# Performance work log

Hardware: AMD Instinct MI355X
Metric: run time of the kernel (lower is better)

## Reference

```python
import jax, jax.numpy as jnp
import numpy as np

B, S, E, H = 2, 2048, 1024, 16
D = E // H  # head_dim = 64


def setup_inputs() -> dict:
    key = jax.random.key(0)
    ks = jax.random.split(key, 5)
    return {
        "hidden_states": jax.random.normal(ks[0], (B, S, E), jnp.float32),
        "c_attn_w": jax.random.normal(ks[1], (E, 3 * E), jnp.float32) * 0.02,
        "c_attn_b": jnp.zeros((3 * E,), jnp.float32),
        "c_proj_w": jax.random.normal(ks[2], (E, E), jnp.float32) * 0.02,
        "c_proj_b": jnp.zeros((E,), jnp.float32),
    }


def reference(hidden_states, c_attn_w, c_attn_b, c_proj_w, c_proj_b):
    # Conv1D: x @ w + b -> qkv [B, S, 3E]
    qkv = hidden_states @ c_attn_w + c_attn_b
    q, k, v = jnp.split(qkv, 3, axis=-1)
    # [B, H, S, D]
    q = q.reshape(B, S, H, D).transpose(0, 2, 1, 3)
    k = k.reshape(B, S, H, D).transpose(0, 2, 1, 3)
    v = v.reshape(B, S, H, D).transpose(0, 2, 1, 3)
    # scores [B, H, S, S], scaled by sqrt(head_dim)
    scores = jnp.einsum("bhqd,bhkd->bhqk", q, k) / jnp.sqrt(jnp.asarray(D, q.dtype))
    causal = jnp.tril(jnp.ones((S, S), bool))  # [S, S]
    mask_value = jnp.finfo(scores.dtype).min
    scores = jnp.where(causal, scores, mask_value)
    attn = jax.nn.softmax(scores, axis=-1)
    # attn @ V -> [B, H, S, D] -> [B, S, E]
    out = jnp.einsum("bhqk,bhkd->bhqd", attn, v)
    out = out.transpose(0, 2, 1, 3).reshape(B, S, E)
    return out @ c_proj_w + c_proj_b
```

## Files before the change

kernel.cpp:

```cpp
#include <hip/hip_runtime.h>

using bf16 = __bf16;
typedef __bf16 bf16x8 __attribute__((ext_vector_type(8)));
typedef __bf16 bf16x4 __attribute__((ext_vector_type(4)));
typedef float  f32x4  __attribute__((ext_vector_type(4)));

#define MFMA16(a, b, c) __builtin_amdgcn_mfma_f32_16x16x32_bf16((a), (b), (c), 0, 0, 0)

static constexpr int S = 2048, E = 1024;
static constexpr float CSCALE = 0.18033688011112042f;

__device__ __forceinline__ void gld16(const bf16* g, bf16* l) {
    __builtin_amdgcn_global_load_lds((const __attribute__((address_space(1))) unsigned*)g,
                                     (__attribute__((address_space(3))) unsigned*)l, 16, 0, 0);
}

__global__ __launch_bounds__(256) void k_prep(const float* __restrict__ hs, const float* __restrict__ w0,
                                              const float* __restrict__ w1, bf16* __restrict__ A0,
                                              bf16* __restrict__ Wt0, bf16* __restrict__ Wt1) {
    __shared__ float tile[32][33];
    const int bx = blockIdx.x;
    if (bx < 4096) {
        int i = (bx * 256 + threadIdx.x) * 4;
        float4 v = *(const float4*)(hs + i);
        bf16x4 o = { (bf16)v.x, (bf16)v.y, (bf16)v.z, (bf16)v.w };
        *(bf16x4*)(A0 + i) = o;
        return;
    }
    const float* in;
    bf16* outp;
    int K, N, nb, kb;
    if (bx < 4096 + 3072) {
        int j = bx - 4096; in = w0; outp = Wt0; K = 1024; N = 3072; nb = j % 96; kb = j / 96;
    } else {
        int j = bx - 7168; in = w1; outp = Wt1; K = 1024; N = 1024; nb = j % 32; kb = j / 32;
    }
    const int bxx = nb * 32, byy = kb * 32;
    const int tx = threadIdx.x & 31, ty = threadIdx.x >> 5;
#pragma unroll
    for (int i = 0; i < 32; i += 8)
        tile[ty + i][tx] = in[(long)(byy + ty + i) * N + bxx + tx];
    __syncthreads();
#pragma unroll
    for (int i = 0; i < 32; i += 8)
        outp[(long)(bxx + ty + i) * K + byy + tx] = (bf16)tile[tx][ty + i];
}

template <bool OUT_F32>
__global__ __launch_bounds__(256) void k_gemm_bt(const bf16* __restrict__ A, const bf16* __restrict__ Bt,
                                                 const float* __restrict__ bias, void* __restrict__ Cout,
                                                 int Mm, int Nn, int Kk, int scale_cols, float scale) {
    const int bm = blockIdx.x * 128;
    const int bn = blockIdx.y * 128;
    const int tid = threadIdx.x;
    const int w = tid >> 6, lane = tid & 63;
    const int wm = (w >> 1) * 64, wn = (w & 1) * 64;
    const int col = lane & 15, quad = lane >> 4;

    __shared__ bf16 sA[128 * 32];
    __shared__ bf16 sB[128 * 32];

    const int c0 = w * 128 + lane;
    const int r0 = c0 >> 2, s0 = c0 & 3;
    const int r1 = (c0 + 64) >> 2, s1 = (c0 + 64) & 3;
    const bf16* pA0 = A + (long)(bm + r0) * Kk + s0 * 8;
    const bf16* pA1 = A + (long)(bm + r1) * Kk + s1 * 8;
    const bf16* pB0 = Bt + (long)(bn + r0) * Kk + s0 * 8;
    const bf16* pB1 = Bt + (long)(bn + r1) * Kk + s1 * 8;
    bf16* lA0 = sA + w * 1024;
    bf16* lA1 = sA + w * 1024 + 512;
    bf16* lB0 = sB + w * 1024;
    bf16* lB1 = sB + w * 1024 + 512;

    f32x4 acc[4][4] = {};

    for (int k0 = 0; k0 < Kk; k0 += 32) {
        __syncthreads();
        gld16(pA0 + k0, lA0);
        gld16(pA1 + k0, lA1);
        gld16(pB0 + k0, lB0);
        gld16(pB1 + k0, lB1);
        __syncthreads();
        bf16x8 af[4], bfr[4];
#pragma unroll
        for (int mt = 0; mt < 4; mt++) af[mt] = *(const bf16x8*)(sA + (wm + mt * 16 + col) * 32 + quad * 8);
#pragma unroll
        for (int nt = 0; nt < 4; nt++) bfr[nt] = *(const bf16x8*)(sB + (wn + nt * 16 + col) * 32 + quad * 8);
#pragma unroll
        for (int mt = 0; mt < 4; mt++)
#pragma unroll
            for (int nt = 0; nt < 4; nt++)
                acc[mt][nt] = MFMA16(af[mt], bfr[nt], acc[mt][nt]);
    }

#pragma unroll
    for (int mt = 0; mt < 4; mt++) {
        const int gr = bm + wm + mt * 16 + quad * 4;
#pragma unroll
        for (int nt = 0; nt < 4; nt++) {
            const int gc = bn + wn + nt * 16 + col;
            const float bv = bias[gc];
            const float sc = (gc < scale_cols) ? scale : 1.0f;
#pragma unroll
            for (int r = 0; r < 4; r++) {
                float vv = (acc[mt][nt][r] + bv) * sc;
                if (OUT_F32) ((float*)Cout)[(long)(gr + r) * Nn + gc] = vv;
                else         ((bf16*)Cout)[(long)(gr + r) * Nn + gc] = (bf16)vv;
            }
        }
    }
}

__global__ __launch_bounds__(256) void k_gemm_bt64(const bf16* __restrict__ A, const bf16* __restrict__ Bt,
                                                    const float* __restrict__ bias, float* __restrict__ Cout,
                                                    int Mm, int Nn, int Kk) {
    const int bm = blockIdx.x * 64;
    const int bn = blockIdx.y * 128;
    const int tid = threadIdx.x;
    const int w = tid >> 6, lane = tid & 63;
    const int wm = (w >> 1) * 32, wn = (w & 1) * 64;
    const int col = lane & 15, quad = lane >> 4;

    __shared__ bf16 sA[64 * 32];
    __shared__ bf16 sB[128 * 32];

    const int ca = w * 64 + lane;
    const int ra = ca >> 2, sa = ca & 3;
    const int c0 = w * 128 + lane;
    const int r0 = c0 >> 2, s0 = c0 & 3;
    const int r1 = (c0 + 64) >> 2, s1 = (c0 + 64) & 3;
    const bf16* pA0 = A + (long)(bm + ra) * Kk + sa * 8;
    const bf16* pB0 = Bt + (long)(bn + r0) * Kk + s0 * 8;
    const bf16* pB1 = Bt + (long)(bn + r1) * Kk + s1 * 8;
    bf16* lA0 = sA + w * 512;
    bf16* lB0 = sB + w * 1024;
    bf16* lB1 = sB + w * 1024 + 512;

    f32x4 acc[2][4] = {};

    for (int k0 = 0; k0 < Kk; k0 += 32) {
        __syncthreads();
        gld16(pA0 + k0, lA0);
        gld16(pB0 + k0, lB0);
        gld16(pB1 + k0, lB1);
        __syncthreads();
        bf16x8 af[2], bfr[4];
#pragma unroll
        for (int mt = 0; mt < 2; mt++) af[mt] = *(const bf16x8*)(sA + (wm + mt * 16 + col) * 32 + quad * 8);
#pragma unroll
        for (int nt = 0; nt < 4; nt++) bfr[nt] = *(const bf16x8*)(sB + (wn + nt * 16 + col) * 32 + quad * 8);
#pragma unroll
        for (int mt = 0; mt < 2; mt++)
#pragma unroll
            for (int nt = 0; nt < 4; nt++)
                acc[mt][nt] = MFMA16(af[mt], bfr[nt], acc[mt][nt]);
    }

#pragma unroll
    for (int mt = 0; mt < 2; mt++) {
        const int gr = bm + wm + mt * 16 + quad * 4;
#pragma unroll
        for (int nt = 0; nt < 4; nt++) {
            const int gc = bn + wn + nt * 16 + col;
            const float bv = bias[gc];
#pragma unroll
            for (int r = 0; r < 4; r++)
                Cout[(long)(gr + r) * Nn + gc] = acc[mt][nt][r] + bv;
        }
    }
}

__global__ __launch_bounds__(256) void k_attn(const bf16* __restrict__ qkv, bf16* __restrict__ out) {
    const int L = blockIdx.x;
    const int bh = L & 31;
    const int t = L >> 5;
    const int qt = (t < 8) ? (15 - t) : (t - 8);
    const int b = bh >> 4, h = bh & 15;
    const int tid = threadIdx.x;
    const int w = tid >> 6, lane = tid & 63;
    const int col = lane & 15, quad = lane >> 4;
    const int q0 = qt * 128;
    const int nkt = 2 * qt + 2;

    __shared__ bf16 sK[2][64 * 72];
    __shared__ bf16 sVt[2][64 * 80];
    __shared__ bf16 sP[4][32 * 72];

    const long base = (long)b * S * 3072;
    const int ko = E + h * 64, vo = 2 * E + h * 64;

    bf16x8 bq[2][2];
#pragma unroll
    for (int qg = 0; qg < 2; qg++) {
        const bf16* qp = qkv + base + (long)(q0 + w * 32 + qg * 16 + col) * 3072 + h * 64 + quad * 8;
        bq[qg][0] = *(const bf16x8*)(qp);
        bq[qg][1] = *(const bf16x8*)(qp + 32);
    }

    const int krow = tid >> 2, kcol = (tid & 3) * 16;
    const int vkk = (tid & 31) * 2, vd0 = (tid >> 5) * 4;
    const bf16* kgp = qkv + base + (long)krow * 3072 + ko + kcol;
    const bf16* vgp = qkv + base + (long)vkk * 3072 + vo + vd0;
    bf16* pw = sP[w];

    bf16x8 kr0 = *(const bf16x8*)(kgp);
    bf16x8 kr1 = *(const bf16x8*)(kgp + 8);
    ushort4 va0 = *(const ushort4*)(vgp);
    ushort4 vb0 = *(const ushort4*)(vgp + 3072);
    ushort4 va1 = *(const ushort4*)(vgp + 32);
    ushort4 vb1 = *(const ushort4*)(vgp + 3072 + 32);

    float m_[2] = { -1e30f, -1e30f }, l_[2] = { 0.f, 0.f };
    f32x4 o[2][4] = {};

    int buf = 0;
#pragma unroll 1
    for (int kt = 0; kt < nkt; kt++) {
        bf16* bK = sK[buf];
        bf16* bV = sVt[buf];
        buf ^= 1;
        *(bf16x8*)(bK + krow * 72 + kcol) = kr0;
        *(bf16x8*)(bK + krow * 72 + kcol + 8) = kr1;
        *(unsigned*)(bV + (vd0 + 0) * 80 + vkk) = (unsigned)va0.x | ((unsigned)vb0.x << 16);
        *(unsigned*)(bV + (vd0 + 1) * 80 + vkk) = (unsigned)va0.y | ((unsigned)vb0.y << 16);
        *(unsigned*)(bV + (vd0 + 2) * 80 + vkk) = (unsigned)va0.z | ((unsigned)vb0.z << 16);
        *(unsigned*)(bV + (vd0 + 3) * 80 + vkk) = (unsigned)va0.w | ((unsigned)vb0.w << 16);
        *(unsigned*)(bV + (vd0 + 32) * 80 + vkk) = (unsigned)va1.x | ((unsigned)vb1.x << 16);
        *(unsigned*)(bV + (vd0 + 33) * 80 + vkk) = (unsigned)va1.y | ((unsigned)vb1.y << 16);
        *(unsigned*)(bV + (vd0 + 34) * 80 + vkk) = (unsigned)va1.z | ((unsigned)vb1.z << 16);
        *(unsigned*)(bV + (vd0 + 35) * 80 + vkk) = (unsigned)va1.w | ((unsigned)vb1.w << 16);
        __syncthreads();

        if (kt + 1 < nkt) {
            const long noff = (long)(kt + 1) * 64 * 3072;
            kr0 = *(const bf16x8*)(kgp + noff);
            kr1 = *(const bf16x8*)(kgp + noff + 8);
            va0 = *(const ushort4*)(vgp + noff);
            vb0 = *(const ushort4*)(vgp + noff + 3072);
            va1 = *(const ushort4*)(vgp + noff + 32);
            vb1 = *(const ushort4*)(vgp + noff + 3072 + 32);
        }

        f32x4 s[2][4];
#pragma unroll
        for (int mt = 0; mt < 4; mt++) {
            const bf16* kp = bK + (mt * 16 + col) * 72 + quad * 8;
            const bf16x8 ka0 = *(const bf16x8*)(kp);
            const bf16x8 ka1 = *(const bf16x8*)(kp + 32);
#pragma unroll
            for (int qg = 0; qg < 2; qg++) {
                f32x4 z = {};
                z = MFMA16(ka0, bq[qg][0], z);
                z = MFMA16(ka1, bq[qg][1], z);
                s[qg][mt] = z;
            }
        }
        if (kt >= 2 * qt) {
#pragma unroll
            for (int qg = 0; qg < 2; qg++) {
                const int qrow = q0 + w * 32 + qg * 16 + col;
#pragma unroll
                for (int mt = 0; mt < 4; mt++)
#pragma unroll
                    for (int r = 0; r < 4; r++)
                        if (kt * 64 + mt * 16 + quad * 4 + r > qrow) s[qg][mt][r] = -1e30f;
            }
        }
#pragma unroll
        for (int qg = 0; qg < 2; qg++) {
            float cm = -1e30f;
#pragma unroll
            for (int mt = 0; mt < 4; mt++)
#pragma unroll
                for (int r = 0; r < 4; r++) cm = fmaxf(cm, s[qg][mt][r]);
            cm = fmaxf(cm, __shfl_xor(cm, 16));
            cm = fmaxf(cm, __shfl_xor(cm, 32));
            const float mnew = fmaxf(m_[qg], cm);
            const float alpha = __builtin_amdgcn_exp2f(m_[qg] - mnew);
            m_[qg] = mnew;
            float rs = 0.f;
#pragma unroll
            for (int mt = 0; mt < 4; mt++)
#pragma unroll
                for (int r = 0; r < 4; r++) {
                    float pe = __builtin_amdgcn_exp2f(s[qg][mt][r] - mnew);
                    s[qg][mt][r] = pe;
                    rs += pe;
                }
            l_[qg] = l_[qg] * alpha + rs;
#pragma unroll
            for (int dt = 0; dt < 4; dt++)
#pragma unroll
                for (int r = 0; r < 4; r++) o[qg][dt][r] *= alpha;
#pragma unroll
            for (int mt = 0; mt < 4; mt++) {
                bf16x4 pk = { (bf16)s[qg][mt][0], (bf16)s[qg][mt][1],
                              (bf16)s[qg][mt][2], (bf16)s[qg][mt][3] };
                *(bf16x4*)(pw + (qg * 16 + col) * 72 + mt * 16 + quad * 4) = pk;
            }
        }
#pragma unroll
        for (int ks = 0; ks < 2; ks++) {
            bf16x8 vf[4];
#pragma unroll
            for (int dt = 0; dt < 4; dt++)
                vf[dt] = *(const bf16x8*)(bV + (dt * 16 + col) * 80 + ks * 32 + quad * 8);
#pragma unroll
            for (int qg = 0; qg < 2; qg++) {
                bf16x8 ap = *(const bf16x8*)(pw + (qg * 16 + col) * 72 + ks * 32 + quad * 8);
#pragma unroll
                for (int dt = 0; dt < 4; dt++)
                    o[qg][dt] = MFMA16(vf[dt], ap, o[qg][dt]);
            }
        }
    }

#pragma unroll
    for (int qg = 0; qg < 2; qg++) {
        float lt = l_[qg];
        lt += __shfl_xor(lt, 16);
        lt += __shfl_xor(lt, 32);
        const float li = 1.f / lt;
        bf16* op = out + (long)(b * S + q0 + w * 32 + qg * 16 + col) * E + h * 64 + quad * 4;
#pragma unroll
        for (int dt = 0; dt < 4; dt++) {
            bf16x4 ov = { (bf16)(o[qg][dt][0] * li), (bf16)(o[qg][dt][1] * li),
                          (bf16)(o[qg][dt][2] * li), (bf16)(o[qg][dt][3] * li) };
            *(bf16x4*)(op + dt * 16) = ov;
        }
    }
}

extern "C" void kernel_launch(void* const* d_in, const int* in_sizes, int n_in,
                              void* d_out, int out_size, void* d_ws, size_t ws_size,
                              hipStream_t stream) {
    const float* hs = (const float*)d_in[0];
    const float* w0 = (const float*)d_in[1];
    const float* b0 = (const float*)d_in[2];
    const float* w1 = (const float*)d_in[3];
    const float* b1 = (const float*)d_in[4];
    float* outp = (float*)d_out;

    char* ws = (char*)d_ws;
    bf16* A0   = (bf16*)(ws);
    bf16* Wt0  = (bf16*)(ws + 8388608);
    bf16* Wt1  = (bf16*)(ws + 14680064);
    bf16* qkv  = (bf16*)(ws + 16777216);
    bf16* attn = (bf16*)(ws + 41943040);

    k_prep<<<8192, 256, 0, stream>>>(hs, w0, w1, A0, Wt0, Wt1);
    k_gemm_bt<false><<<dim3(32, 24), 256, 0, stream>>>(A0, Wt0, b0, qkv, 4096, 3072, 1024, 1024, CSCALE);
    k_attn<<<512, 256, 0, stream>>>(qkv, attn);
    k_gemm_bt64<<<dim3(64, 8), 256, 0, stream>>>(attn, Wt1, b1, outp, 4096, 1024, 1024);
}
```

Before: 187.2 us.

## Emit head-major K and transposed V from QKV GEMM; attention reads global directly

The QKV GEMM epilogue now writes Q (pre-scaled), head-major K and transposed V into separate buffers. The attention kernel drops its shared-memory K/V staging, double buffering and block-wide syncs, and loads K and V fragments straight from global memory. Each wave now handles its own 32-row query tile independently, with a fresh causal ordering, so waves in a block no longer share K/V tiles. This removes LDS traffic and barriers but relies on L1/L2 for reuse and increases redundant global loads per block. The GEMM epilogue also writes K and V with a more scattered pattern.

```diff
diff --git a/kernel.cpp b/kernel.cpp
--- a/kernel.cpp
+++ b/kernel.cpp
@@ -46,12 +46,12 @@
         outp[(long)(bxx + ty + i) * K + byy + tx] = (bf16)tile[tx][ty + i];
 }
 
-template <bool OUT_F32>
-__global__ __launch_bounds__(256) void k_gemm_bt(const bf16* __restrict__ A, const bf16* __restrict__ Bt,
-                                                 const float* __restrict__ bias, void* __restrict__ Cout,
-                                                 int Mm, int Nn, int Kk, int scale_cols, float scale) {
+__global__ __launch_bounds__(256) void k_gemm_qkv(const bf16* __restrict__ A, const bf16* __restrict__ Bt,
+                                                  const float* __restrict__ bias, bf16* __restrict__ Qs,
+                                                  bf16* __restrict__ Kh, bf16* __restrict__ Vt, int Kk) {
     const int bm = blockIdx.x * 128;
     const int bn = blockIdx.y * 128;
+    const int Nn = 3072;
     const int tid = threadIdx.x;
     const int w = tid >> 6, lane = tid & 63;
     const int wm = (w >> 1) * 64, wn = (w & 1) * 64;
@@ -96,16 +96,26 @@
 #pragma unroll
     for (int mt = 0; mt < 4; mt++) {
         const int gr = bm + wm + mt * 16 + quad * 4;
+        const int bb = gr >> 11, ss = gr & 2047;
 #pragma unroll
         for (int nt = 0; nt < 4; nt++) {
             const int gc = bn + wn + nt * 16 + col;
             const float bv = bias[gc];
-            const float sc = (gc < scale_cols) ? scale : 1.0f;
-#pragma unroll
-            for (int r = 0; r < 4; r++) {
-                float vv = (acc[mt][nt][r] + bv) * sc;
-                if (OUT_F32) ((float*)Cout)[(long)(gr + r) * Nn + gc] = vv;
-                else         ((bf16*)Cout)[(long)(gr + r) * Nn + gc] = (bf16)vv;
+            const int seg = gc >> 10;
+            if (seg == 0) {
+#pragma unroll
+                for (int r = 0; r < 4; r++)
+                    Qs[(long)(gr + r) * 1024 + gc] = (bf16)((acc[mt][nt][r] + bv) * CSCALE);
+            } else if (seg == 1) {
+                const int d = gc - 1024, h = d >> 6, dd = d & 63;
+                bf16* kp = Kh + ((long)(bb * 16 + h) << 17) + (long)ss * 64 + dd;
+#pragma unroll
+                for (int r = 0; r < 4; r++) kp[r * 64] = (bf16)(acc[mt][nt][r] + bv);
+            } else {
+                const int d = gc - 2048, h = d >> 6, dd = d & 63;
+                bf16x4 vv = { (bf16)(acc[mt][nt][0] + bv), (bf16)(acc[mt][nt][1] + bv),
+                              (bf16)(acc[mt][nt][2] + bv), (bf16)(acc[mt][nt][3] + bv) };
+                *(bf16x4*)(Vt + ((long)(bb * 16 + h) << 17) + (long)dd * 2048 + ss) = vv;
             }
         }
     }
@@ -170,81 +180,41 @@
     }
 }
 
-__global__ __launch_bounds__(256) void k_attn(const bf16* __restrict__ qkv, bf16* __restrict__ out) {
-    const int L = blockIdx.x;
-    const int bh = L & 31;
-    const int t = L >> 5;
-    const int qt = (t < 8) ? (15 - t) : (t - 8);
-    const int b = bh >> 4, h = bh & 15;
+__global__ __launch_bounds__(256) void k_attn(const bf16* __restrict__ Qs, const bf16* __restrict__ Kh,
+                                              const bf16* __restrict__ Vt, bf16* __restrict__ out) {
+    const int bx = blockIdx.x;
+    const int bh = bx & 31;
     const int tid = threadIdx.x;
     const int w = tid >> 6, lane = tid & 63;
     const int col = lane & 15, quad = lane >> 4;
-    const int q0 = qt * 128;
-    const int nkt = 2 * qt + 2;
-
-    __shared__ bf16 sK[2][64 * 72];
-    __shared__ bf16 sVt[2][64 * 80];
+    const int t = 63 - ((bx >> 5) * 4 + w);
+    const int b = bh >> 4, h = bh & 15;
+    const int q0 = t * 32;
+    const int nkt = (t >> 1) + 1;
+
     __shared__ bf16 sP[4][32 * 72];
-
-    const long base = (long)b * S * 3072;
-    const int ko = E + h * 64, vo = 2 * E + h * 64;
+    bf16* pw = sP[w];
+
+    const bf16* kbase = Kh + ((long)bh << 17);
+    const bf16* vbase = Vt + ((long)bh << 17);
 
     bf16x8 bq[2][2];
 #pragma unroll
     for (int qg = 0; qg < 2; qg++) {
-        const bf16* qp = qkv + base + (long)(q0 + w * 32 + qg * 16 + col) * 3072 + h * 64 + quad * 8;
+        const bf16* qp = Qs + (long)(b * S + q0 + qg * 16 + col) * E + h * 64 + quad * 8;
         bq[qg][0] = *(const bf16x8*)(qp);
         bq[qg][1] = *(const bf16x8*)(qp + 32);
     }
-
-    const int krow = tid >> 2, kcol = (tid & 3) * 16;
-    const int vkk = (tid & 31) * 2, vd0 = (tid >> 5) * 4;
-    const bf16* kgp = qkv + base + (long)krow * 3072 + ko + kcol;
-    const bf16* vgp = qkv + base + (long)vkk * 3072 + vo + vd0;
-    bf16* pw = sP[w];
-
-    bf16x8 kr0 = *(const bf16x8*)(kgp);
-    bf16x8 kr1 = *(const bf16x8*)(kgp + 8);
-    ushort4 va0 = *(const ushort4*)(vgp);
-    ushort4 vb0 = *(const ushort4*)(vgp + 3072);
-    ushort4 va1 = *(const ushort4*)(vgp + 32);
-    ushort4 vb1 = *(const ushort4*)(vgp + 3072 + 32);
-
     float m_[2] = { -1e30f, -1e30f }, l_[2] = { 0.f, 0.f };
     f32x4 o[2][4] = {};
 
-    int buf = 0;
 #pragma unroll 1
     for (int kt = 0; kt < nkt; kt++) {
-        bf16* bK = sK[buf];
-        bf16* bV = sVt[buf];
-        buf ^= 1;
-        *(bf16x8*)(bK + krow * 72 + kcol) = kr0;
-        *(bf16x8*)(bK + krow * 72 + kcol + 8) = kr1;
-        *(unsigned*)(bV + (vd0 + 0) * 80 + vkk) = (unsigned)va0.x | ((unsigned)vb0.x << 16);
-        *(unsigned*)(bV + (vd0 + 1) * 80 + vkk) = (unsigned)va0.y | ((unsigned)vb0.y << 16);
-        *(unsigned*)(bV + (vd0 + 2) * 80 + vkk) = (unsigned)va0.z | ((unsigned)vb0.z << 16);
-        *(unsigned*)(bV + (vd0 + 3) * 80 + vkk) = (unsigned)va0.w | ((unsigned)vb0.w << 16);
-        *(unsigned*)(bV + (vd0 + 32) * 80 + vkk) = (unsigned)va1.x | ((unsigned)vb1.x << 16);
-        *(unsigned*)(bV + (vd0 + 33) * 80 + vkk) = (unsigned)va1.y | ((unsigned)vb1.y << 16);
-        *(unsigned*)(bV + (vd0 + 34) * 80 + vkk) = (unsigned)va1.z | ((unsigned)vb1.z << 16);
-        *(unsigned*)(bV + (vd0 + 35) * 80 + vkk) = (unsigned)va1.w | ((unsigned)vb1.w << 16);
-        __syncthreads();
-
-        if (kt + 1 < nkt) {
-            const long noff = (long)(kt + 1) * 64 * 3072;
-            kr0 = *(const bf16x8*)(kgp + noff);
-            kr1 = *(const bf16x8*)(kgp + noff + 8);
-            va0 = *(const ushort4*)(vgp + noff);
-            vb0 = *(const ushort4*)(vgp + noff + 3072);
-            va1 = *(const ushort4*)(vgp + noff + 32);
-            vb1 = *(const ushort4*)(vgp + noff + 3072 + 32);
-        }
-
+        const int k0 = kt * 64;
         f32x4 s[2][4];
 #pragma unroll
         for (int mt = 0; mt < 4; mt++) {
-            const bf16* kp = bK + (mt * 16 + col) * 72 + quad * 8;
+            const bf16* kp = kbase + (long)(k0 + mt * 16 + col) * 64 + quad * 8;
             const bf16x8 ka0 = *(const bf16x8*)(kp);
             const bf16x8 ka1 = *(const bf16x8*)(kp + 32);
 #pragma unroll
@@ -255,15 +225,15 @@
                 s[qg][mt] = z;
             }
         }
-        if (kt >= 2 * qt) {
+        if (kt == nkt - 1) {
 #pragma unroll
             for (int qg = 0; qg < 2; qg++) {
-                const int qrow = q0 + w * 32 + qg * 16 + col;
+                const int qrow = q0 + qg * 16 + col;
 #pragma unroll
                 for (int mt = 0; mt < 4; mt++)
 #pragma unroll
                     for (int r = 0; r < 4; r++)
-                        if (kt * 64 + mt * 16 + quad * 4 + r > qrow) s[qg][mt][r] = -1e30f;
+                        if (k0 + mt * 16 + quad * 4 + r > qrow) s[qg][mt][r] = -1e30f;
             }
         }
 #pragma unroll
@@ -301,16 +271,16 @@
         }
 #pragma unroll
         for (int ks = 0; ks < 2; ks++) {
-            bf16x8 vf[4];
-#pragma unroll
-            for (int dt = 0; dt < 4; dt++)
-                vf[dt] = *(const bf16x8*)(bV + (dt * 16 + col) * 80 + ks * 32 + quad * 8);
-#pragma unroll
-            for (int qg = 0; qg < 2; qg++) {
-                bf16x8 ap = *(const bf16x8*)(pw + (qg * 16 + col) * 72 + ks * 32 + quad * 8);
-#pragma unroll
-                for (int dt = 0; dt < 4; dt++)
-                    o[qg][dt] = MFMA16(vf[dt], ap, o[qg][dt]);
+            bf16x8 ap[2];
+#pragma unroll
+            for (int qg = 0; qg < 2; qg++)
+                ap[qg] = *(const bf16x8*)(pw + (qg * 16 + col) * 72 + ks * 32 + quad * 8);
+#pragma unroll
+            for (int dt = 0; dt < 4; dt++) {
+                const bf16x8 vf = *(const bf16x8*)(vbase + (long)(dt * 16 + col) * 2048 + k0 + ks * 32 + quad * 8);
+#pragma unroll
+                for (int qg = 0; qg < 2; qg++)
+                    o[qg][dt] = MFMA16(vf, ap[qg], o[qg][dt]);
             }
         }
     }
@@ -321,7 +291,7 @@
         lt += __shfl_xor(lt, 16);
         lt += __shfl_xor(lt, 32);
         const float li = 1.f / lt;
-        bf16* op = out + (long)(b * S + q0 + w * 32 + qg * 16 + col) * E + h * 64 + quad * 4;
+        bf16* op = out + (long)(b * S + q0 + qg * 16 + col) * E + h * 64 + quad * 4;
 #pragma unroll
         for (int dt = 0; dt < 4; dt++) {
             bf16x4 ov = { (bf16)(o[qg][dt][0] * li), (bf16)(o[qg][dt][1] * li),
@@ -342,14 +312,16 @@
     float* outp = (float*)d_out;
 
     char* ws = (char*)d_ws;
-    bf16* A0   = (bf16*)(ws);
-    bf16* Wt0  = (bf16*)(ws + 8388608);
-    bf16* Wt1  = (bf16*)(ws + 14680064);
-    bf16* qkv  = (bf16*)(ws + 16777216);
-    bf16* attn = (bf16*)(ws + 41943040);
+    bf16* A0    = (bf16*)(ws);
+    bf16* Wt0   = (bf16*)(ws + 8388608);
+    bf16* Wt1   = (bf16*)(ws + 14680064);
+    bf16* Qs    = (bf16*)(ws + 16777216);
+    bf16* Kh    = (bf16*)(ws + 25165824);
+    bf16* Vt    = (bf16*)(ws + 33554432);
+    bf16* attnO = (bf16*)(ws + 41943040);
 
     k_prep<<<8192, 256, 0, stream>>>(hs, w0, w1, A0, Wt0, Wt1);
-    k_gemm_bt<false><<<dim3(32, 24), 256, 0, stream>>>(A0, Wt0, b0, qkv, 4096, 3072, 1024, 1024, CSCALE);
-    k_attn<<<512, 256, 0, stream>>>(qkv, attn);
-    k_gemm_bt64<<<dim3(64, 8), 256, 0, stream>>>(attn, Wt1, b1, outp, 4096, 1024, 1024);
-}
+    k_gemm_qkv<<<dim3(32, 24), 256, 0, stream>>>(A0, Wt0, b0, Qs, Kh, Vt, 1024);
+    k_attn<<<512, 256, 0, stream>>>(Qs, Kh, Vt, attnO);
+    k_gemm_bt64<<<dim3(64, 8), 256, 0, stream>>>(attnO, Wt1, b1, outp, 4096, 1024, 1024);
+}
```

Result: slower. 240.1 us (+28.3%).
